# Kernel tuning notes

Measured on AMD Instinct MI355X. Metric: run time of the kernel, lower is better.

## Reference

```python
import jax, jax.numpy as jnp
import numpy as np

B, T, D, H, C = 32, 2048, 256, 256, 128


def setup_inputs() -> dict:
    key = jax.random.key(0)
    ks = jax.random.split(key, 4)
    s = 0.05  # small init to avoid gate saturation
    return {
        "x": jax.random.normal(ks[0], (B, T, D), jnp.float32),
        "W_gate": jax.random.normal(ks[1], (D + H, 2 * H), jnp.float32) * s,
        "b_gate": jnp.ones((2 * H,), jnp.float32),  # TF GRUCell gate bias init = 1.0
        "W_cand": jax.random.normal(ks[2], (D + H, H), jnp.float32) * s,
        "b_cand": jnp.zeros((H,), jnp.float32),
        "W_proj": jax.random.normal(ks[3], (H, C), jnp.float32) * s,
        "b_proj": jnp.zeros((C,), jnp.float32),
    }


def reference(x, W_gate, b_gate, W_cand, b_cand, W_proj, b_proj):
    # Split the TF concat([x, h]) kernels into input and recurrent parts.
    Wx_g, Wh_g = W_gate[:D], W_gate[D:]
    Wx_c, Wh_c = W_cand[:D], W_cand[D:]
    # Batch the input-to-hidden GEMMs over all timesteps at once.
    gx = jnp.einsum('btd,dg->btg', x, Wx_g) + b_gate   # [B,T,2H]
    cx = jnp.einsum('btd,dh->bth', x, Wx_c) + b_cand   # [B,T,H]

    def step(h, inp):
        gxt, cxt = inp                                  # [B,2H], [B,H]
        gates = jax.nn.sigmoid(gxt + h @ Wh_g)          # r, u gates
        r, u = gates[:, :H], gates[:, H:]
        c = jnp.tanh(cxt + (r * h) @ Wh_c)              # candidate
        h_new = u * h + (1.0 - u) * c                   # TF GRUCell update
        return h_new, h_new

    h0 = jnp.zeros((x.shape[0], H), x.dtype)
    gx_t = jnp.swapaxes(gx, 0, 1)                       # time-major for scan
    cx_t = jnp.swapaxes(cx, 0, 1)
    _, ys = jax.lax.scan(step, h0, (gx_t, cx_t))        # [T,B,H]
    # Per-timestep linear + sigmoid projection (one batched GEMM).
    out = jax.nn.sigmoid(jnp.einsum('tbh,hc->tbc', ys, W_proj) + b_proj)
    return jnp.swapaxes(out, 0, 1)                      # [B,T,C]
```

## Files before the change

### kernel.cpp

```cpp
#include <hip/hip_runtime.h>
#include <cstdint>
#include <cstddef>

#define BB 32
#define TT 2048
#define DD 256
#define HH 256
#define CC 128
#define GG 512

#if defined(__has_builtin)
#  if __has_builtin(__builtin_amdgcn_fdot2_f32_bf16)
#    define HAVE_BF16_DOT2 1
#  endif
#endif
#ifndef HAVE_BF16_DOT2
#  define HAVE_BF16_DOT2 0
#endif

#if HAVE_BF16_DOT2
typedef __bf16 bf16x2_t __attribute__((ext_vector_type(2)));
#endif

__device__ __forceinline__ float bflo(uint32_t w) { return __uint_as_float(w << 16); }
__device__ __forceinline__ float bfhi(uint32_t w) { return __uint_as_float(w & 0xffff0000u); }

__device__ __forceinline__ float dot2bf(uint32_t w, uint32_t h, float acc) {
#if HAVE_BF16_DOT2
  return __builtin_amdgcn_fdot2_f32_bf16(__builtin_bit_cast(bf16x2_t, w),
                                         __builtin_bit_cast(bf16x2_t, h),
                                         acc, false);
#else
  acc = fmaf(bflo(w), bflo(h), acc);
  acc = fmaf(bfhi(w), bfhi(h), acc);
  return acc;
#endif
}

__device__ __forceinline__ uint16_t f2bf(float x) {
  uint32_t u = __float_as_uint(x);
  uint32_t r = (u + 0x7fffu + ((u >> 16) & 1u)) >> 16;
  return (uint16_t)r;
}

__device__ __forceinline__ uint32_t pkbf(float a, float b) {
  return (uint32_t)f2bf(a) | ((uint32_t)f2bf(b) << 16);
}

__global__ void prep_kernel(const float* __restrict__ Wg, const float* __restrict__ bg,
                            const float* __restrict__ Wc, const float* __restrict__ bc,
                            const float* __restrict__ Wp,
                            float* __restrict__ Bm, float* __restrict__ bias,
                            uint32_t* __restrict__ Whg2, uint32_t* __restrict__ Whc2,
                            uint32_t* __restrict__ Wp2) {
  int i = blockIdx.x * 256 + threadIdx.x;
  if (i < 196608) {
    int k = i / 768, n = i % 768;
    Bm[i] = (n < GG) ? Wg[k * GG + n] : Wc[k * HH + (n - GG)];
    return;
  }
  int j = i - 196608;
  if (j < 768) {
    bias[j] = (j < GG) ? bg[j] : bc[j - GG];
    return;
  }
  int a = i - 197376;
  if (a < 65536) {
    int k2 = a >> 9, jj = a & 511;
    Whg2[a] = pkbf(Wg[(DD + 2 * k2) * GG + jj], Wg[(DD + 2 * k2 + 1) * GG + jj]);
    return;
  }
  int c2 = i - 262912;
  if (c2 < 32768) {
    int k2 = c2 >> 8, jj = c2 & 255;
    Whc2[c2] = pkbf(Wc[(DD + 2 * k2) * HH + jj], Wc[(DD + 2 * k2 + 1) * HH + jj]);
    return;
  }
  int p2 = i - 295680;
  if (p2 < 16384) {
    int k2 = p2 >> 7, jj = p2 & 127;
    Wp2[p2] = pkbf(Wp[(2 * k2) * CC + jj], Wp[(2 * k2 + 1) * CC + jj]);
  }
}

__global__ __launch_bounds__(256) void gemm_in(const float* __restrict__ A,
                                               const float* __restrict__ Bm,
                                               const float* __restrict__ bias,
                                               float* __restrict__ Cm) {
  __shared__ __align__(16) float As[16][65];
  __shared__ __align__(16) float Bs[16][64];
  const int tidx = threadIdx.x;
  const int tx = tidx & 15;
  const int ty = tidx >> 4;
  const int m0 = blockIdx.y * 64;
  const int n0 = blockIdx.x * 64;
  float acc[4][4] = {};

  for (int k0 = 0; k0 < DD; k0 += 16) {
    {
      int r = tidx >> 2;
      int c = (tidx & 3) * 4;
      float4 av = *(const float4*)(A + (size_t)(m0 + r) * DD + k0 + c);
      As[c + 0][r] = av.x; As[c + 1][r] = av.y; As[c + 2][r] = av.z; As[c + 3][r] = av.w;
    }
    {
      int r = tidx >> 6;
      int cc = tidx & 63;
      #pragma unroll
      for (int i = 0; i < 4; i++)
        Bs[r + i * 4][cc] = Bm[(size_t)(k0 + r + i * 4) * 768 + n0 + cc];
    }
    __syncthreads();
    #pragma unroll
    for (int kk = 0; kk < 16; kk++) {
      float a[4], bb[4];
      #pragma unroll
      for (int i = 0; i < 4; i++) a[i] = As[kk][ty * 4 + i];
      #pragma unroll
      for (int jj = 0; jj < 4; jj++) bb[jj] = Bs[kk][tx * 4 + jj];
      #pragma unroll
      for (int i = 0; i < 4; i++)
        #pragma unroll
        for (int jj = 0; jj < 4; jj++)
          acc[i][jj] = fmaf(a[i], bb[jj], acc[i][jj]);
    }
    __syncthreads();
  }
  float4 bv = *(const float4*)&bias[n0 + tx * 4];
  #pragma unroll
  for (int i = 0; i < 4; i++) {
    int m = m0 + ty * 4 + i;
    float4 o;
    o.x = acc[i][0] + bv.x; o.y = acc[i][1] + bv.y;
    o.z = acc[i][2] + bv.z; o.w = acc[i][3] + bv.w;
    *(float4*)(Cm + (size_t)m * 768 + n0 + tx * 4) = o;
  }
}

__global__ __launch_bounds__(512, 2) void rnn_scan_reg(
    const float* __restrict__ gxc,
    const uint32_t* __restrict__ Whg2,
    const uint32_t* __restrict__ Whc2,
    const uint32_t* __restrict__ Wp2,
    const float* __restrict__ bproj,
    float* __restrict__ out) {
  __shared__ __align__(16) uint32_t s_h2[HH / 2];
  __shared__ __align__(16) float    s_hf[HH];
  __shared__ __align__(16) uint32_t s_rh2[HH / 2];
  __shared__ __align__(16) float    s_u[HH];
  __shared__ __align__(16) float    s_p[512];

  const int tid = threadIdx.x;
  const int b = blockIdx.x;
  const int jc = tid & 255, kh = tid >> 8;
  const int j3 = tid & 127, q = tid >> 7;

  uint32_t wg[128];
  #pragma unroll
  for (int i = 0; i < 128; i++) wg[i] = Whg2[i * 512 + tid];
  uint32_t wc[64];
  #pragma unroll
  for (int i = 0; i < 64; i++) wc[i] = Whc2[(kh * 64 + i) * 256 + jc];
  uint32_t wpj[32];
  #pragma unroll
  for (int i = 0; i < 32; i++) wpj[i] = Wp2[(q * 32 + i) * 128 + j3];

  if (tid < HH) s_hf[tid] = 0.f;
  if (tid < HH / 2) s_h2[tid] = 0u;

  const float* gx_b = gxc + (size_t)b * TT * 768;
  float* out_b = out + (size_t)b * TT * CC;

  float bp = (tid < CC) ? bproj[tid] : 0.f;
  float gv  = gx_b[tid];
  float cxv = gx_b[GG + jc];

  __syncthreads();

  for (int t = 0; t < TT; t++) {
    int tn = (t + 1 < TT) ? (t + 1) : (TT - 1);
    const float* gx_n = gx_b + (size_t)tn * 768;
    float gv_n  = gx_n[tid];
    float cx_n  = gx_n[GG + jc];

    float acc = gv;
    #pragma unroll
    for (int k2 = 0; k2 < 128; k2 += 4) {
      uint4 hh = *(const uint4*)&s_h2[k2];
      acc = dot2bf(wg[k2 + 0], hh.x, acc);
      acc = dot2bf(wg[k2 + 1], hh.y, acc);
      acc = dot2bf(wg[k2 + 2], hh.z, acc);
      acc = dot2bf(wg[k2 + 3], hh.w, acc);
    }
    float g = 1.f / (1.f + __expf(-acc));
    if (tid < HH) {
      ((uint16_t*)s_rh2)[tid] = f2bf(g * s_hf[tid]);
    } else {
      s_u[tid - HH] = g;
    }
    __syncthreads();

    {
      float acc2 = 0.f;
      #pragma unroll
      for (int i = 0; i < 64; i += 4) {
        uint4 rr = *(const uint4*)&s_rh2[kh * 64 + i];
        acc2 = dot2bf(wc[i + 0], rr.x, acc2);
        acc2 = dot2bf(wc[i + 1], rr.y, acc2);
        acc2 = dot2bf(wc[i + 2], rr.z, acc2);
        acc2 = dot2bf(wc[i + 3], rr.w, acc2);
      }
      s_p[kh * 256 + jc] = acc2;
    }
    __syncthreads();

    if (tid < HH) {
      float pre = cxv + s_p[tid] + s_p[256 + tid];
      float e = __expf(-2.f * fabsf(pre));
      float tm = (1.f - e) / (1.f + e);
      float c = copysignf(tm, pre);
      float u = s_u[tid];
      float hf = s_hf[tid];
      float hn = u * hf + (1.f - u) * c;
      s_hf[tid] = hn;
      ((uint16_t*)s_h2)[tid] = f2bf(hn);
    }
    __syncthreads();

    {
      float acc3 = 0.f;
      #pragma unroll
      for (int i = 0; i < 32; i += 4) {
        uint4 hh = *(const uint4*)&s_h2[q * 32 + i];
        acc3 = dot2bf(wpj[i + 0], hh.x, acc3);
        acc3 = dot2bf(wpj[i + 1], hh.y, acc3);
        acc3 = dot2bf(wpj[i + 2], hh.z, acc3);
        acc3 = dot2bf(wpj[i + 3], hh.w, acc3);
      }
      s_p[q * 128 + j3] = acc3;
    }
    __syncthreads();

    if (tid < CC) {
      float pre = bp + s_p[tid] + s_p[128 + tid] + s_p[256 + tid] + s_p[384 + tid];
      out_b[(size_t)t * CC + tid] = 1.f / (1.f + __expf(-pre));
    }

    gv = gv_n; cxv = cx_n;
  }
}

extern "C" void kernel_launch(void* const* d_in, const int* in_sizes, int n_in,
                              void* d_out, int out_size, void* d_ws, size_t ws_size,
                              hipStream_t stream) {
  const float* x  = (const float*)d_in[0];
  const float* Wg = (const float*)d_in[1];
  const float* bg = (const float*)d_in[2];
  const float* Wc = (const float*)d_in[3];
  const float* bc = (const float*)d_in[4];
  const float* Wp = (const float*)d_in[5];
  const float* bp = (const float*)d_in[6];
  float* out = (float*)d_out;

  char* w = (char*)d_ws;
  float*    gxc  = (float*)   (w);
  float*    Bm   = (float*)   (w + 201326592ull);
  float*    bias = (float*)   (w + 202113024ull);
  uint32_t* Whg2 = (uint32_t*)(w + 202116096ull);
  uint32_t* Whc2 = (uint32_t*)(w + 202378240ull);
  uint32_t* Wp2  = (uint32_t*)(w + 202509312ull);

  prep_kernel<<<1219, 256, 0, stream>>>(Wg, bg, Wc, bc, Wp, Bm, bias, Whg2, Whc2, Wp2);
  gemm_in<<<dim3(12, 1024), 256, 0, stream>>>(x, Bm, bias, gxc);
  rnn_scan_reg<<<BB, 512, 0, stream>>>(gxc, Whg2, Whc2, Wp2, bp, out);
}
```

Baseline: 3.891 ms.

## Split each batch recurrence across four workgroups with global-memory flag sync

```diff
diff --git a/kernel.cpp b/kernel.cpp
--- a/kernel.cpp
+++ b/kernel.cpp
@@ -47,12 +47,19 @@
   return (uint32_t)f2bf(a) | ((uint32_t)f2bf(b) << 16);
 }
 
+__device__ __forceinline__ float sigm(float x) { return 1.f / (1.f + __expf(-x)); }
+__device__ __forceinline__ float tanh_f(float x) {
+  float e = __expf(-2.f * fabsf(x));
+  float t = (1.f - e) / (1.f + e);
+  return copysignf(t, x);
+}
+
 __global__ void prep_kernel(const float* __restrict__ Wg, const float* __restrict__ bg,
                             const float* __restrict__ Wc, const float* __restrict__ bc,
                             const float* __restrict__ Wp,
                             float* __restrict__ Bm, float* __restrict__ bias,
                             uint32_t* __restrict__ Whg2, uint32_t* __restrict__ Whc2,
-                            uint32_t* __restrict__ Wp2) {
+                            uint32_t* __restrict__ Wp2, uint32_t* __restrict__ fh) {
   int i = blockIdx.x * 256 + threadIdx.x;
   if (i < 196608) {
     int k = i / 768, n = i % 768;
@@ -80,7 +87,10 @@
   if (p2 < 16384) {
     int k2 = p2 >> 7, jj = p2 & 127;
     Wp2[p2] = pkbf(Wp[(2 * k2) * CC + jj], Wp[(2 * k2 + 1) * CC + jj]);
-  }
+    return;
+  }
+  int f = i - 312064;
+  if (f < 2048) fh[f] = 0u;
 }
 
 __global__ __launch_bounds__(256) void gemm_in(const float* __restrict__ A,
@@ -98,17 +108,17 @@
 
   for (int k0 = 0; k0 < DD; k0 += 16) {
     {
-      int r = tidx >> 2;
+      int rr = tidx >> 2;
       int c = (tidx & 3) * 4;
-      float4 av = *(const float4*)(A + (size_t)(m0 + r) * DD + k0 + c);
-      As[c + 0][r] = av.x; As[c + 1][r] = av.y; As[c + 2][r] = av.z; As[c + 3][r] = av.w;
+      float4 av = *(const float4*)(A + (size_t)(m0 + rr) * DD + k0 + c);
+      As[c + 0][rr] = av.x; As[c + 1][rr] = av.y; As[c + 2][rr] = av.z; As[c + 3][rr] = av.w;
     }
     {
-      int r = tidx >> 6;
+      int rr = tidx >> 6;
       int cc = tidx & 63;
       #pragma unroll
       for (int i = 0; i < 4; i++)
-        Bs[r + i * 4][cc] = Bm[(size_t)(k0 + r + i * 4) * 768 + n0 + cc];
+        Bs[rr + i * 4][cc] = Bm[(size_t)(k0 + rr + i * 4) * 768 + n0 + cc];
     }
     __syncthreads();
     #pragma unroll
@@ -137,116 +147,181 @@
   }
 }
 
-__global__ __launch_bounds__(512, 2) void rnn_scan_reg(
+__global__ __launch_bounds__(512, 2) void rnn_scan_g4(
     const float* __restrict__ gxc,
     const uint32_t* __restrict__ Whg2,
     const uint32_t* __restrict__ Whc2,
     const uint32_t* __restrict__ Wp2,
     const float* __restrict__ bproj,
-    float* __restrict__ out) {
-  __shared__ __align__(16) uint32_t s_h2[HH / 2];
-  __shared__ __align__(16) float    s_hf[HH];
-  __shared__ __align__(16) uint32_t s_rh2[HH / 2];
-  __shared__ __align__(16) float    s_u[HH];
-  __shared__ __align__(16) float    s_p[512];
-
+    float* __restrict__ out,
+    uint32_t* __restrict__ h_x,
+    uint32_t* __restrict__ fh) {
+  __shared__ __align__(16) uint32_t s_h2[128];
+  __shared__ __align__(16) uint32_t s_rh2[128];
+  __shared__ __align__(16) float s_pr[4][256];
+  __shared__ __align__(16) float s_pu[8][64];
+  __shared__ __align__(16) float s_pp[16][32];
+  __shared__ __align__(16) float s_pc[8][64];
+  __shared__ __align__(16) float s_u[64];
+  __shared__ __align__(16) float s_hfl[64];
+
+  const int bid = blockIdx.x;
+  const int b = bid & 31;
+  const int r = bid >> 5;
   const int tid = threadIdx.x;
-  const int b = blockIdx.x;
-  const int jc = tid & 255, kh = tid >> 8;
-  const int j3 = tid & 127, q = tid >> 7;
-
-  uint32_t wg[128];
-  #pragma unroll
-  for (int i = 0; i < 128; i++) wg[i] = Whg2[i * 512 + tid];
-  uint32_t wc[64];
-  #pragma unroll
-  for (int i = 0; i < 64; i++) wc[i] = Whc2[(kh * 64 + i) * 256 + jc];
-  uint32_t wpj[32];
-  #pragma unroll
-  for (int i = 0; i < 32; i++) wpj[i] = Wp2[(q * 32 + i) * 128 + j3];
-
-  if (tid < HH) s_hf[tid] = 0.f;
-  if (tid < HH / 2) s_h2[tid] = 0u;
+
+  const int jpr  = tid & 127;
+  const int ksp4 = tid >> 7;
+  const int ju   = tid & 63;
+  const int ksp8 = tid >> 6;
+  const int u2   = ksp8 & 1;
+  const int jp   = tid & 31;
+  const int ksp16 = tid >> 5;
+  const int m4   = ksp16 & 3;
+
+  uint32_t wr0[32], wr1[32];
+  #pragma unroll
+  for (int i = 0; i < 32; i++) {
+    wr0[i] = Whg2[(32 * ksp4 + i) * 512 + 2 * jpr];
+    wr1[i] = Whg2[(32 * ksp4 + i) * 512 + 2 * jpr + 1];
+  }
+  uint32_t wu[16];
+  #pragma unroll
+  for (int i = 0; i < 16; i++) wu[i] = Whg2[(16 * ksp8 + i) * 512 + 256 + 64 * r + ju];
+  uint32_t wc[16];
+  #pragma unroll
+  for (int i = 0; i < 16; i++) wc[i] = Whc2[(16 * ksp8 + i) * 256 + 64 * r + ju];
+  uint32_t wp[8];
+  #pragma unroll
+  for (int i = 0; i < 8; i++) wp[i] = Wp2[(8 * ksp16 + i) * 128 + 32 * r + jp];
+
+  if (tid < 128) s_h2[tid] = 0u;
+  if (tid < 64) s_hfl[tid] = 0.f;
 
   const float* gx_b = gxc + (size_t)b * TT * 768;
   float* out_b = out + (size_t)b * TT * CC;
-
-  float bp = (tid < CC) ? bproj[tid] : 0.f;
-  float gv  = gx_b[tid];
-  float cxv = gx_b[GG + jc];
+  const float bpv = (tid >= 192 && tid < 224) ? bproj[32 * r + (tid - 192)] : 0.f;
 
   __syncthreads();
 
-  for (int t = 0; t < TT; t++) {
-    int tn = (t + 1 < TT) ? (t + 1) : (TT - 1);
-    const float* gx_n = gx_b + (size_t)tn * 768;
-    float gv_n  = gx_n[tid];
-    float cx_n  = gx_n[GG + jc];
-
-    float acc = gv;
+  for (int t = 0; t <= TT; t++) {
+    const int tg = (t < TT) ? t : (TT - 1);
+    const float* gx_t = gx_b + (size_t)tg * 768;
+
+    float gxr0 = 0.f, gxr1 = 0.f, gxu = 0.f, cx0 = 0.f, cx1 = 0.f;
+    if (tid < 128) {
+      float2 gp = *(const float2*)&gx_t[2 * tid];
+      gxr0 = gp.x; gxr1 = gp.y;
+      if (tid < 32) {
+        float2 cp = *(const float2*)&gx_t[GG + 64 * r + 2 * tid];
+        cx0 = cp.x; cx1 = cp.y;
+      }
+    } else if (tid < 192) {
+      gxu = gx_t[256 + 64 * r + (tid - 128)];
+    }
+
+    float ar0 = 0.f, ar1 = 0.f, au = 0.f, ap = 0.f;
     #pragma unroll
-    for (int k2 = 0; k2 < 128; k2 += 4) {
-      uint4 hh = *(const uint4*)&s_h2[k2];
-      acc = dot2bf(wg[k2 + 0], hh.x, acc);
-      acc = dot2bf(wg[k2 + 1], hh.y, acc);
-      acc = dot2bf(wg[k2 + 2], hh.z, acc);
-      acc = dot2bf(wg[k2 + 3], hh.w, acc);
-    }
-    float g = 1.f / (1.f + __expf(-acc));
-    if (tid < HH) {
-      ((uint16_t*)s_rh2)[tid] = f2bf(g * s_hf[tid]);
-    } else {
-      s_u[tid - HH] = g;
-    }
-    __syncthreads();
+    for (int i2 = 0; i2 < 8; i2++) {
+      uint4 hq = *(const uint4*)&s_h2[32 * ksp4 + 4 * i2];
+      ar0 = dot2bf(wr0[4 * i2 + 0], hq.x, ar0);
+      ar0 = dot2bf(wr0[4 * i2 + 1], hq.y, ar0);
+      ar0 = dot2bf(wr0[4 * i2 + 2], hq.z, ar0);
+      ar0 = dot2bf(wr0[4 * i2 + 3], hq.w, ar0);
+      ar1 = dot2bf(wr1[4 * i2 + 0], hq.x, ar1);
+      ar1 = dot2bf(wr1[4 * i2 + 1], hq.y, ar1);
+      ar1 = dot2bf(wr1[4 * i2 + 2], hq.z, ar1);
+      ar1 = dot2bf(wr1[4 * i2 + 3], hq.w, ar1);
+      if ((i2 >> 2) == u2) {
+        au = dot2bf(wu[4 * (i2 & 3) + 0], hq.x, au);
+        au = dot2bf(wu[4 * (i2 & 3) + 1], hq.y, au);
+        au = dot2bf(wu[4 * (i2 & 3) + 2], hq.z, au);
+        au = dot2bf(wu[4 * (i2 & 3) + 3], hq.w, au);
+      }
+      if (2 * m4 == i2) {
+        ap = dot2bf(wp[0], hq.x, ap);
+        ap = dot2bf(wp[1], hq.y, ap);
+        ap = dot2bf(wp[2], hq.z, ap);
+        ap = dot2bf(wp[3], hq.w, ap);
+      } else if (2 * m4 + 1 == i2) {
+        ap = dot2bf(wp[4], hq.x, ap);
+        ap = dot2bf(wp[5], hq.y, ap);
+        ap = dot2bf(wp[6], hq.z, ap);
+        ap = dot2bf(wp[7], hq.w, ap);
+      }
+    }
+    *(float2*)&s_pr[ksp4][2 * jpr] = make_float2(ar0, ar1);
+    s_pu[ksp8][ju] = au;
+    s_pp[ksp16][jp] = ap;
+    __syncthreads();
+
+    if (tid < 128) {
+      float v0 = s_pr[0][2 * tid] + s_pr[1][2 * tid] + s_pr[2][2 * tid] + s_pr[3][2 * tid] + gxr0;
+      float v1 = s_pr[0][2 * tid + 1] + s_pr[1][2 * tid + 1] + s_pr[2][2 * tid + 1] + s_pr[3][2 * tid + 1] + gxr1;
+      float r0 = sigm(v0), r1 = sigm(v1);
+      uint32_t hw = s_h2[tid];
+      s_rh2[tid] = pkbf(r0 * bflo(hw), r1 * bfhi(hw));
+    } else if (tid < 192) {
+      int j = tid - 128;
+      float a = gxu;
+      #pragma unroll
+      for (int k = 0; k < 8; k++) a += s_pu[k][j];
+      s_u[j] = sigm(a);
+    } else if (tid < 224 && t > 0) {
+      int j = tid - 192;
+      float a = bpv;
+      #pragma unroll
+      for (int k = 0; k < 16; k++) a += s_pp[k][j];
+      out_b[(size_t)(t - 1) * CC + 32 * r + j] = sigm(a);
+    }
+    __syncthreads();
+
+    if (t == TT) break;
 
     {
-      float acc2 = 0.f;
-      #pragma unroll
-      for (int i = 0; i < 64; i += 4) {
-        uint4 rr = *(const uint4*)&s_rh2[kh * 64 + i];
-        acc2 = dot2bf(wc[i + 0], rr.x, acc2);
-        acc2 = dot2bf(wc[i + 1], rr.y, acc2);
-        acc2 = dot2bf(wc[i + 2], rr.z, acc2);
-        acc2 = dot2bf(wc[i + 3], rr.w, acc2);
+      float ac = 0.f;
+      #pragma unroll
+      for (int i2 = 0; i2 < 4; i2++) {
+        uint4 rq = *(const uint4*)&s_rh2[16 * ksp8 + 4 * i2];
+        ac = dot2bf(wc[4 * i2 + 0], rq.x, ac);
+        ac = dot2bf(wc[4 * i2 + 1], rq.y, ac);
+        ac = dot2bf(wc[4 * i2 + 2], rq.z, ac);
+        ac = dot2bf(wc[4 * i2 + 3], rq.w, ac);
       }
-      s_p[kh * 256 + jc] = acc2;
-    }
-    __syncthreads();
-
-    if (tid < HH) {
-      float pre = cxv + s_p[tid] + s_p[256 + tid];
-      float e = __expf(-2.f * fabsf(pre));
-      float tm = (1.f - e) / (1.f + e);
-      float c = copysignf(tm, pre);
-      float u = s_u[tid];
-      float hf = s_hf[tid];
-      float hn = u * hf + (1.f - u) * c;
-      s_hf[tid] = hn;
-      ((uint16_t*)s_h2)[tid] = f2bf(hn);
-    }
-    __syncthreads();
-
-    {
-      float acc3 = 0.f;
-      #pragma unroll
-      for (int i = 0; i < 32; i += 4) {
-        uint4 hh = *(const uint4*)&s_h2[q * 32 + i];
-        acc3 = dot2bf(wpj[i + 0], hh.x, acc3);
-        acc3 = dot2bf(wpj[i + 1], hh.y, acc3);
-        acc3 = dot2bf(wpj[i + 2], hh.z, acc3);
-        acc3 = dot2bf(wpj[i + 3], hh.w, acc3);
-      }
-      s_p[q * 128 + j3] = acc3;
-    }
-    __syncthreads();
-
-    if (tid < CC) {
-      float pre = bp + s_p[tid] + s_p[128 + tid] + s_p[256 + tid] + s_p[384 + tid];
-      out_b[(size_t)t * CC + tid] = 1.f / (1.f + __expf(-pre));
-    }
-
-    gv = gv_n; cxv = cx_n;
+      s_pc[ksp8][ju] = ac;
+    }
+    __syncthreads();
+
+    if (tid < 32) {
+      int c0 = 2 * tid, c1 = 2 * tid + 1;
+      float a0 = cx0, a1 = cx1;
+      #pragma unroll
+      for (int k = 0; k < 8; k++) { a0 += s_pc[k][c0]; a1 += s_pc[k][c1]; }
+      float cc0 = tanh_f(a0), cc1 = tanh_f(a1);
+      float u0 = s_u[c0], u1 = s_u[c1];
+      float h0 = s_hfl[c0], h1 = s_hfl[c1];
+      float hn0 = u0 * h0 + (1.f - u0) * cc0;
+      float hn1 = u1 * h1 + (1.f - u1) * cc1;
+      s_hfl[c0] = hn0; s_hfl[c1] = hn1;
+      uint32_t hwv = pkbf(hn0, hn1);
+      __hip_atomic_store(&h_x[((size_t)(t & 1) * 32 + b) * 128 + 32 * r + tid], hwv,
+                         __ATOMIC_RELAXED, __HIP_MEMORY_SCOPE_AGENT);
+    }
+    if (tid == 0) {
+      __builtin_amdgcn_fence(__ATOMIC_RELEASE, "agent");
+      __hip_atomic_store(&fh[(b * 4 + r) * 16], (uint32_t)(t + 1),
+                         __ATOMIC_RELAXED, __HIP_MEMORY_SCOPE_AGENT);
+    }
+
+    if (tid < 128) {
+      const uint32_t tgt = (uint32_t)(t + 1);
+      uint32_t* fp = &fh[(b * 4 + (tid >> 5)) * 16];
+      while (__hip_atomic_load(fp, __ATOMIC_RELAXED, __HIP_MEMORY_SCOPE_AGENT) < tgt) {}
+      __builtin_amdgcn_fence(__ATOMIC_ACQUIRE, "agent");
+      s_h2[tid] = __hip_atomic_load(&h_x[((size_t)(t & 1) * 32 + b) * 128 + tid],
+                                    __ATOMIC_RELAXED, __HIP_MEMORY_SCOPE_AGENT);
+    }
+    __syncthreads();
   }
 }
 
@@ -269,8 +344,10 @@
   uint32_t* Whg2 = (uint32_t*)(w + 202116096ull);
   uint32_t* Whc2 = (uint32_t*)(w + 202378240ull);
   uint32_t* Wp2  = (uint32_t*)(w + 202509312ull);
-
-  prep_kernel<<<1219, 256, 0, stream>>>(Wg, bg, Wc, bc, Wp, Bm, bias, Whg2, Whc2, Wp2);
+  uint32_t* h_x  = (uint32_t*)(w + 202574848ull);
+  uint32_t* fh   = (uint32_t*)(w + 202607616ull);
+
+  prep_kernel<<<1227, 256, 0, stream>>>(Wg, bg, Wc, bc, Wp, Bm, bias, Whg2, Whc2, Wp2, fh);
   gemm_in<<<dim3(12, 1024), 256, 0, stream>>>(x, Bm, bias, gxc);
-  rnn_scan_reg<<<BB, 512, 0, stream>>>(gxc, Whg2, Whc2, Wp2, bp, out);
-}
+  rnn_scan_g4<<<128, 512, 0, stream>>>(gxc, Whg2, Whc2, Wp2, bp, out, h_x, fh);
+}
```

Result: slower. 8.904 ms (+128.9%).

## Move output projection out of recurrent scan into separate parallel kernel

Applied to the files above, without the earlier changes.

```diff
diff --git a/kernel.cpp b/kernel.cpp
--- a/kernel.cpp
+++ b/kernel.cpp
@@ -45,6 +45,13 @@
 
 __device__ __forceinline__ uint32_t pkbf(float a, float b) {
   return (uint32_t)f2bf(a) | ((uint32_t)f2bf(b) << 16);
+}
+
+__device__ __forceinline__ float sigm(float x) { return 1.f / (1.f + __expf(-x)); }
+__device__ __forceinline__ float tanh_f(float x) {
+  float e = __expf(-2.f * fabsf(x));
+  float t = (1.f - e) / (1.f + e);
+  return copysignf(t, x);
 }
 
 __global__ void prep_kernel(const float* __restrict__ Wg, const float* __restrict__ bg,
@@ -98,17 +105,17 @@
 
   for (int k0 = 0; k0 < DD; k0 += 16) {
     {
-      int r = tidx >> 2;
+      int rr = tidx >> 2;
       int c = (tidx & 3) * 4;
-      float4 av = *(const float4*)(A + (size_t)(m0 + r) * DD + k0 + c);
-      As[c + 0][r] = av.x; As[c + 1][r] = av.y; As[c + 2][r] = av.z; As[c + 3][r] = av.w;
+      float4 av = *(const float4*)(A + (size_t)(m0 + rr) * DD + k0 + c);
+      As[c + 0][rr] = av.x; As[c + 1][rr] = av.y; As[c + 2][rr] = av.z; As[c + 3][rr] = av.w;
     }
     {
-      int r = tidx >> 6;
+      int rr = tidx >> 6;
       int cc = tidx & 63;
       #pragma unroll
       for (int i = 0; i < 4; i++)
-        Bs[r + i * 4][cc] = Bm[(size_t)(k0 + r + i * 4) * 768 + n0 + cc];
+        Bs[rr + i * 4][cc] = Bm[(size_t)(k0 + rr + i * 4) * 768 + n0 + cc];
     }
     __syncthreads();
     #pragma unroll
@@ -137,23 +144,19 @@
   }
 }
 
-__global__ __launch_bounds__(512, 2) void rnn_scan_reg(
-    const float* __restrict__ gxc,
-    const uint32_t* __restrict__ Whg2,
-    const uint32_t* __restrict__ Whc2,
-    const uint32_t* __restrict__ Wp2,
-    const float* __restrict__ bproj,
-    float* __restrict__ out) {
-  __shared__ __align__(16) uint32_t s_h2[HH / 2];
-  __shared__ __align__(16) float    s_hf[HH];
-  __shared__ __align__(16) uint32_t s_rh2[HH / 2];
-  __shared__ __align__(16) float    s_u[HH];
-  __shared__ __align__(16) float    s_p[512];
+__global__ __launch_bounds__(512) __attribute__((amdgpu_waves_per_eu(2, 2)))
+void rnn_scan32(float* __restrict__ gxc,
+                const uint32_t* __restrict__ Whg2,
+                const uint32_t* __restrict__ Whc2) {
+  __shared__ __align__(16) uint32_t s_h2[128];
+  __shared__ __align__(16) uint32_t s_rh2[128];
+  __shared__ __align__(16) float s_pc[2][256];
+  __shared__ __align__(16) float s_u[256];
+  __shared__ __align__(16) float s_hf[256];
 
   const int tid = threadIdx.x;
   const int b = blockIdx.x;
   const int jc = tid & 255, kh = tid >> 8;
-  const int j3 = tid & 127, q = tid >> 7;
 
   uint32_t wg[128];
   #pragma unroll
@@ -161,27 +164,21 @@
   uint32_t wc[64];
   #pragma unroll
   for (int i = 0; i < 64; i++) wc[i] = Whc2[(kh * 64 + i) * 256 + jc];
-  uint32_t wpj[32];
-  #pragma unroll
-  for (int i = 0; i < 32; i++) wpj[i] = Wp2[(q * 32 + i) * 128 + j3];
-
-  if (tid < HH) s_hf[tid] = 0.f;
-  if (tid < HH / 2) s_h2[tid] = 0u;
-
-  const float* gx_b = gxc + (size_t)b * TT * 768;
-  float* out_b = out + (size_t)b * TT * CC;
-
-  float bp = (tid < CC) ? bproj[tid] : 0.f;
-  float gv  = gx_b[tid];
-  float cxv = gx_b[GG + jc];
+
+  if (tid < 128) s_h2[tid] = 0u;
+  if (tid < 256) s_hf[tid] = 0.f;
+
+  float* gx_b = gxc + (size_t)b * TT * 768;
+  float gv = gx_b[tid];
+  float cxv = (tid < 256) ? gx_b[GG + tid] : 0.f;
 
   __syncthreads();
 
   for (int t = 0; t < TT; t++) {
-    int tn = (t + 1 < TT) ? (t + 1) : (TT - 1);
+    const int tn = (t + 1 < TT) ? (t + 1) : (TT - 1);
     const float* gx_n = gx_b + (size_t)tn * 768;
-    float gv_n  = gx_n[tid];
-    float cx_n  = gx_n[GG + jc];
+    float gv_n = gx_n[tid];
+    float cx_n = (tid < 256) ? gx_n[GG + tid] : 0.f;
 
     float acc = gv;
     #pragma unroll
@@ -192,61 +189,85 @@
       acc = dot2bf(wg[k2 + 2], hh.z, acc);
       acc = dot2bf(wg[k2 + 3], hh.w, acc);
     }
-    float g = 1.f / (1.f + __expf(-acc));
-    if (tid < HH) {
+    float g = sigm(acc);
+    if (tid < 256) {
       ((uint16_t*)s_rh2)[tid] = f2bf(g * s_hf[tid]);
     } else {
-      s_u[tid - HH] = g;
+      s_u[tid - 256] = g;
     }
     __syncthreads();
 
     {
-      float acc2 = 0.f;
+      float ac = 0.f;
       #pragma unroll
       for (int i = 0; i < 64; i += 4) {
-        uint4 rr = *(const uint4*)&s_rh2[kh * 64 + i];
-        acc2 = dot2bf(wc[i + 0], rr.x, acc2);
-        acc2 = dot2bf(wc[i + 1], rr.y, acc2);
-        acc2 = dot2bf(wc[i + 2], rr.z, acc2);
-        acc2 = dot2bf(wc[i + 3], rr.w, acc2);
+        uint4 rq = *(const uint4*)&s_rh2[kh * 64 + i];
+        ac = dot2bf(wc[i + 0], rq.x, ac);
+        ac = dot2bf(wc[i + 1], rq.y, ac);
+        ac = dot2bf(wc[i + 2], rq.z, ac);
+        ac = dot2bf(wc[i + 3], rq.w, ac);
       }
-      s_p[kh * 256 + jc] = acc2;
-    }
-    __syncthreads();
-
-    if (tid < HH) {
-      float pre = cxv + s_p[tid] + s_p[256 + tid];
-      float e = __expf(-2.f * fabsf(pre));
-      float tm = (1.f - e) / (1.f + e);
-      float c = copysignf(tm, pre);
+      s_pc[kh][jc] = ac;
+    }
+    __syncthreads();
+
+    if (tid < 256) {
+      float pre = cxv + s_pc[0][tid] + s_pc[1][tid];
+      float c = tanh_f(pre);
       float u = s_u[tid];
       float hf = s_hf[tid];
       float hn = u * hf + (1.f - u) * c;
       s_hf[tid] = hn;
-      ((uint16_t*)s_h2)[tid] = f2bf(hn);
-    }
-    __syncthreads();
-
-    {
-      float acc3 = 0.f;
-      #pragma unroll
-      for (int i = 0; i < 32; i += 4) {
-        uint4 hh = *(const uint4*)&s_h2[q * 32 + i];
-        acc3 = dot2bf(wpj[i + 0], hh.x, acc3);
-        acc3 = dot2bf(wpj[i + 1], hh.y, acc3);
-        acc3 = dot2bf(wpj[i + 2], hh.z, acc3);
-        acc3 = dot2bf(wpj[i + 3], hh.w, acc3);
-      }
-      s_p[q * 128 + j3] = acc3;
-    }
-    __syncthreads();
-
-    if (tid < CC) {
-      float pre = bp + s_p[tid] + s_p[128 + tid] + s_p[256 + tid] + s_p[384 + tid];
-      out_b[(size_t)t * CC + tid] = 1.f / (1.f + __expf(-pre));
-    }
+      uint16_t hb = f2bf(hn);
+      ((uint16_t*)s_h2)[tid] = hb;
+      ((uint16_t*)(gx_b + (size_t)t * 768 + GG))[tid] = hb;
+    }
+    __syncthreads();
 
     gv = gv_n; cxv = cx_n;
+  }
+}
+
+__global__ __launch_bounds__(512) void proj_out(const uint32_t* __restrict__ gxcu,
+                                                const uint32_t* __restrict__ Wp2,
+                                                const float* __restrict__ bp,
+                                                float* __restrict__ out) {
+  __shared__ uint32_t s_wpT[16384];
+  const int tid = threadIdx.x;
+
+  #pragma unroll
+  for (int i = 0; i < 8; i++) {
+    int q = tid + i * 512;
+    uint4 v = ((const uint4*)Wp2)[q];
+    int k2 = q >> 5;
+    int c0 = (q & 31) * 4;
+    s_wpT[(c0 + 0) * 128 + (k2 ^ (((c0 + 0) & 7) << 2))] = v.x;
+    s_wpT[(c0 + 1) * 128 + (k2 ^ (((c0 + 1) & 7) << 2))] = v.y;
+    s_wpT[(c0 + 2) * 128 + (k2 ^ (((c0 + 2) & 7) << 2))] = v.z;
+    s_wpT[(c0 + 3) * 128 + (k2 ^ (((c0 + 3) & 7) << 2))] = v.w;
+  }
+  __syncthreads();
+
+  const int col = tid & 127;
+  const int rsub = tid >> 7;
+  const float bpc = bp[col];
+  const int base = blockIdx.x * 256;
+  const int cswz = (col & 7) << 2;
+
+  for (int rr = 0; rr < 64; rr++) {
+    int m = base + rr * 4 + rsub;
+    const uint32_t* hrow = gxcu + (size_t)m * 768 + 512;
+    float acc = bpc;
+    #pragma unroll 8
+    for (int i2 = 0; i2 < 32; i2++) {
+      uint4 hq = *(const uint4*)&hrow[4 * i2];
+      uint4 wq = *(const uint4*)&s_wpT[col * 128 + ((4 * i2) ^ cswz)];
+      acc = dot2bf(wq.x, hq.x, acc);
+      acc = dot2bf(wq.y, hq.y, acc);
+      acc = dot2bf(wq.z, hq.z, acc);
+      acc = dot2bf(wq.w, hq.w, acc);
+    }
+    out[(size_t)m * 128 + col] = sigm(acc);
   }
 }
 
@@ -272,5 +293,6 @@
 
   prep_kernel<<<1219, 256, 0, stream>>>(Wg, bg, Wc, bc, Wp, Bm, bias, Whg2, Whc2, Wp2);
   gemm_in<<<dim3(12, 1024), 256, 0, stream>>>(x, Bm, bias, gxc);
-  rnn_scan_reg<<<BB, 512, 0, stream>>>(gxc, Whg2, Whc2, Wp2, bp, out);
-}
+  rnn_scan32<<<BB, 512, 0, stream>>>(gxc, Whg2, Whc2);
+  proj_out<<<256, 512, 0, stream>>>((const uint32_t*)gxc, Wp2, bp, out);
+}
```

Result: faster. 3.720 ms (-4.4%).
